# Kernel tuning notes

Measured on AMD Instinct MI355X. Metric: run time of the kernel, lower is better.

Reference implementation:

```python
import jax, jax.numpy as jnp
import numpy as np

B, L, ENC_IN, C_OUT = 4, 2048, 64, 64
D_MODEL, N_HEADS, D_FF, E_LAYERS = 1024, 16, 4096, 4
CA_K = 5  # ChannelAttention1D kernel: int(|log2(1024)+1|/2)=5 (odd)


def _layer_norm(x, w, b, eps=1e-5):
    m = x.mean(-1, keepdims=True)
    v = ((x - m) ** 2).mean(-1, keepdims=True)
    return (x - m) * jax.lax.rsqrt(v + eps) * w + b


def _flow_attention(q, k, v):
    # q,k,v: [B, L, H, D] -> work in [B, H, L, D]
    q = jax.nn.sigmoid(jnp.swapaxes(q, 1, 2))
    k = jax.nn.sigmoid(jnp.swapaxes(k, 1, 2))
    v = jnp.swapaxes(v, 1, 2)
    eps = 1e-6
    Lq = q.shape[2]
    S = k.shape[2]
    nr = 1.0 / jnp.einsum('bhld,bhd->bhl', q + eps, k.sum(axis=2) + eps)
    nc = 1.0 / jnp.einsum('bhsd,bhd->bhs', k + eps, q.sum(axis=2) + eps)
    nrr = jnp.einsum('bhld,bhd->bhl', q + eps, (k * nc[..., None]).sum(axis=2) + eps)
    ncr = jnp.einsum('bhsd,bhd->bhs', k + eps, (q * nr[..., None]).sum(axis=2) + eps)
    nrr = jax.nn.sigmoid(nrr * (float(Lq) / float(S)))
    ncr = jax.nn.softmax(ncr, axis=-1) * S
    kv = jnp.einsum('bhsd,bhse->bhde', k, v * ncr[..., None])  # [B,H,D,Dv]
    out = jnp.einsum('bhld,bhde->bhle', q, kv) * nr[..., None] * nrr[..., None]
    return jnp.swapaxes(out, 1, 2)  # [B, L, H, Dv]


def _token_embed(x, w):
    # x: [B, L, Cin]; circular conv1d kernel=3, pad=1, no bias
    xt = jnp.swapaxes(x, 1, 2)  # [B, Cin, L]
    xt = jnp.concatenate([xt[..., -1:], xt, xt[..., :1]], axis=-1)
    y = jax.lax.conv_general_dilated(xt, w, (1,), 'VALID',
                                     dimension_numbers=('NCH', 'OIH', 'NCH'))
    return jnp.swapaxes(y, 1, 2)  # [B, L, d_model]


def _channel_att(x, w):
    # x: [B, L, C]; squeeze over L, conv over channel axis, sigmoid gate
    y = x.mean(axis=1, keepdims=True)  # [B, 1, C]
    pad = CA_K // 2
    yp = jnp.pad(y, ((0, 0), (0, 0), (pad, pad)))
    yc = jax.lax.conv_general_dilated(yp, w.reshape(1, 1, CA_K), (1,), 'VALID',
                                      dimension_numbers=('NCH', 'OIH', 'NCH'))
    return x * jax.nn.sigmoid(yc)


def _encoder_layer(x, Wq, bq, Wk, bk, Wv, bv, Wo, bo,
                   ln1w, ln1b, ln2w, ln2b, c1w, c1b, c2w, c2b):
    Bx, Lx, _ = x.shape
    q = (x @ Wq.T + bq).reshape(Bx, Lx, N_HEADS, -1)
    k = (x @ Wk.T + bk).reshape(Bx, Lx, N_HEADS, -1)
    v = (x @ Wv.T + bv).reshape(Bx, Lx, N_HEADS, -1)
    a = _flow_attention(q, k, v).reshape(Bx, Lx, -1)
    a = a @ Wo.T + bo
    x = _layer_norm(x + a, ln1w, ln1b)
    y = jax.nn.relu(jnp.einsum('bld,fd->blf', x, c1w) + c1b)  # conv1 k=1
    y = jnp.einsum('blf,df->bld', y, c2w) + c2b               # conv2 k=1
    return _layer_norm(x + y, ln2w, ln2b)


def setup_inputs() -> dict:
    key = jax.random.key(0)
    ks = jax.random.split(key, 16)
    s = 0.02
    E, D, F = E_LAYERS, D_MODEL, D_FF
    inp = {
        'x': jax.random.normal(ks[0], (B, L, ENC_IN), jnp.float32),
        'tok_conv_w': jax.random.normal(ks[1], (D, ENC_IN, 3), jnp.float32) * s,
        'Wq': jax.random.normal(ks[2], (E, D, D), jnp.float32) * s,
        'bq': jnp.zeros((E, D), jnp.float32),
        'Wk': jax.random.normal(ks[3], (E, D, D), jnp.float32) * s,
        'bk': jnp.zeros((E, D), jnp.float32),
        'Wv': jax.random.normal(ks[4], (E, D, D), jnp.float32) * s,
        'bv': jnp.zeros((E, D), jnp.float32),
        'Wo': jax.random.normal(ks[5], (E, D, D), jnp.float32) * s,
        'bo': jnp.zeros((E, D), jnp.float32),
        'conv1_w': jax.random.normal(ks[6], (E, F, D), jnp.float32) * s,
        'conv1_b': jnp.zeros((E, F), jnp.float32),
        'conv2_w': jax.random.normal(ks[7], (E, D, F), jnp.float32) * s,
        'conv2_b': jnp.zeros((E, D), jnp.float32),
        'ln1_w': jnp.ones((E, D), jnp.float32),
        'ln1_b': jnp.zeros((E, D), jnp.float32),
        'ln2_w': jnp.ones((E, D), jnp.float32),
        'ln2_b': jnp.zeros((E, D), jnp.float32),
        'ca_w': jax.random.normal(ks[8], (E, CA_K), jnp.float32) * 0.2,
        'lnf_w': jnp.ones((D,), jnp.float32),
        'lnf_b': jnp.zeros((D,), jnp.float32),
        'proj_w': jax.random.normal(ks[9], (C_OUT, D), jnp.float32) * s,
        'proj_b': jnp.zeros((C_OUT,), jnp.float32),
    }
    return inp


def reference(x, tok_conv_w, Wq, bq, Wk, bk, Wv, bv, Wo, bo,
              conv1_w, conv1_b, conv2_w, conv2_b,
              ln1_w, ln1_b, ln2_w, ln2_b, ca_w,
              lnf_w, lnf_b, proj_w, proj_b):
    h = _token_embed(x, tok_conv_w)  # dropout = identity (eval)
    for i in range(E_LAYERS):
        h = _encoder_layer(h, Wq[i], bq[i], Wk[i], bk[i], Wv[i], bv[i], Wo[i], bo[i],
                           ln1_w[i], ln1_b[i], ln2_w[i], ln2_b[i],
                           conv1_w[i], conv1_b[i], conv2_w[i], conv2_b[i])
        h = _channel_att(h, ca_w[i])
    # Encoder re-applies the last attention layer after the conv loop (faithful)
    i = E_LAYERS - 1
    h = _encoder_layer(h, Wq[i], bq[i], Wk[i], bk[i], Wv[i], bv[i], Wo[i], bo[i],
                       ln1_w[i], ln1_b[i], ln2_w[i], ln2_b[i],
                       conv1_w[i], conv1_b[i], conv2_w[i], conv2_b[i])
    h = _layer_norm(h, lnf_w, lnf_b)
    return h @ proj_w.T + proj_b
```

## Files before the change

### kernel.cpp

```cpp
#include <hip/hip_runtime.h>
#include <stdint.h>

#define L_SEQ 2048
#define DM 1024
#define NH 16
#define DFF 4096
#define NB 4
#define ROWS (NB * L_SEQ)

typedef __attribute__((ext_vector_type(8))) __bf16 bf16x8;
typedef __attribute__((ext_vector_type(4))) float f32x4;

__device__ __forceinline__ float bf2f(unsigned short u) {
  union { unsigned int i; float f; } x; x.i = ((unsigned int)u) << 16; return x.f;
}
__device__ __forceinline__ unsigned short f2bf(float f) {
  union { float f; unsigned int i; } x; x.f = f;
  unsigned int r = x.i + 0x7FFFu + ((x.i >> 16) & 1u);
  return (unsigned short)(r >> 16);
}

typedef __attribute__((address_space(3))) void lds_void;
typedef const __attribute__((address_space(1))) void gbl_void;

__device__ __forceinline__ void stage16(const void* g, void* ldsbase) {
  __builtin_amdgcn_global_load_lds((gbl_void*)g, (lds_void*)ldsbase, 16, 0, 0);
}

__global__ __launch_bounds__(256)
void gemm_bt(const unsigned short* __restrict__ A,
             const unsigned short* __restrict__ B,
             const float* __restrict__ bias,
             unsigned short* __restrict__ C16,
             float* __restrict__ C32,
             int K, int lda, int ldc, int n_limit, int act)
{
  __shared__ __attribute__((aligned(16))) unsigned short As[128 * 32];
  __shared__ __attribute__((aligned(16))) unsigned short Bs[128 * 32];
  const int tid  = threadIdx.x;
  const int wave = tid >> 6, lane = tid & 63;
  const int wm = (wave & 1) << 6, wn = (wave >> 1) << 6;
  const int l16 = lane & 15, quad = lane >> 4;

  const unsigned short* Ab = A + (size_t)blockIdx.x * 128 * lda;
  const unsigned short* Bb = B + (size_t)blockIdx.y * 128 * K;

  const int srow = (wave << 4) + (lane >> 2);
  const int scol = (lane & 3) << 3;

  f32x4 acc[4][4] = {};

  for (int k0 = 0; k0 < K; k0 += 32) {
    const size_t aoff = (size_t)srow * lda + k0 + scol;
    const size_t boff = (size_t)srow * K   + k0 + scol;
    stage16(Ab + aoff,                    &As[(wave * 16) * 32]);
    stage16(Ab + aoff + (size_t)64 * lda, &As[(wave * 16 + 64) * 32]);
    stage16(Bb + boff,                    &Bs[(wave * 16) * 32]);
    stage16(Bb + boff + (size_t)64 * K,   &Bs[(wave * 16 + 64) * 32]);
    __syncthreads();

    bf16x8 af[4], bfr[4];
#pragma unroll
    for (int mi = 0; mi < 4; mi++)
      af[mi] = *(const bf16x8*)&As[(wm + mi * 16 + l16) * 32 + quad * 8];
#pragma unroll
    for (int ni = 0; ni < 4; ni++)
      bfr[ni] = *(const bf16x8*)&Bs[(wn + ni * 16 + l16) * 32 + quad * 8];
#pragma unroll
    for (int mi = 0; mi < 4; mi++)
#pragma unroll
      for (int ni = 0; ni < 4; ni++)
        acc[mi][ni] = __builtin_amdgcn_mfma_f32_16x16x32_bf16(af[mi], bfr[ni], acc[mi][ni], 0, 0, 0);
    __syncthreads();
  }

  const int row0 = (int)blockIdx.x * 128 + wm + quad * 4;
  const int col0 = (int)blockIdx.y * 128 + wn + l16;
#pragma unroll
  for (int ni = 0; ni < 4; ni++) {
    const int col = col0 + ni * 16;
    if (col >= n_limit) continue;
    const float bv = bias ? bias[col] : 0.0f;
    const bool sig = (act == 2) || (act == 3 && col < 2048);
#pragma unroll
    for (int mi = 0; mi < 4; mi++) {
#pragma unroll
      for (int r = 0; r < 4; r++) {
        const int row = row0 + mi * 16 + r;
        float v = acc[mi][ni][r] + bv;
        if (act == 1) v = fmaxf(v, 0.0f);
        else if (sig) v = 1.0f / (1.0f + __expf(-v));
        if (C32) C32[(size_t)row * ldc + col] = v;
        if (C16) C16[(size_t)row * ldc + col] = f2bf(v);
      }
    }
  }
}


__global__ __launch_bounds__(256)
void fa_sums(const unsigned short* __restrict__ Q, const unsigned short* __restrict__ K,
             int ld, float* __restrict__ ksp, float* __restrict__ qsp)
{
  const int bh = blockIdx.x, chunk = blockIdx.y;
  const size_t base = ((size_t)(bh >> 4) * L_SEQ) * ld + (size_t)(bh & 15) * 64;
  const int t = threadIdx.x, lane = t & 63, wave = t >> 6;
  __shared__ float red[256];
  float ks = 0.f, qs = 0.f;
  const int l0 = chunk * 256 + wave * 64;
  for (int i = 0; i < 64; i++) {
    const size_t idx = base + (size_t)(l0 + i) * ld + lane;
    ks += bf2f(K[idx]);
    qs += bf2f(Q[idx]);
  }
  red[t] = ks; __syncthreads();
  if (t < 64) ksp[(bh * 8 + chunk) * 64 + t] = red[t] + red[t + 64] + red[t + 128] + red[t + 192];
  __syncthreads();
  red[t] = qs; __syncthreads();
  if (t < 64) qsp[(bh * 8 + chunk) * 64 + t] = red[t] + red[t + 64] + red[t + 128] + red[t + 192];
}

__global__ __launch_bounds__(256)
void fa_rows1(const unsigned short* __restrict__ Q, const unsigned short* __restrict__ K,
              int ld, const float* __restrict__ ksp, const float* __restrict__ qsp,
              float* __restrict__ nr, float* __restrict__ t1p, float* __restrict__ t2p)
{
  const int bh = blockIdx.x, chunk = blockIdx.y;
  const size_t base = ((size_t)(bh >> 4) * L_SEQ) * ld + (size_t)(bh & 15) * 64;
  const int t = threadIdx.x, lane = t & 63, wave = t >> 6;
  const float eps = 1e-6f;
  __shared__ float s_kse[64], s_qse[64], red[256];
  if (t < 64) {
    float s = 0.f;
    for (int j = 0; j < 8; j++) s += ksp[(bh * 8 + j) * 64 + t];
    s_kse[t] = s + eps;
  } else if (t < 128) {
    const int d = t - 64;
    float s = 0.f;
    for (int j = 0; j < 8; j++) s += qsp[(bh * 8 + j) * 64 + d];
    s_qse[d] = s + eps;
  }
  __syncthreads();
  const float kse = s_kse[lane], qse = s_qse[lane];
  float t1a = 0.f, t2a = 0.f;
  for (int i = 0; i < 32; i++) {
    const int l = chunk * 128 + wave + 4 * i;
    const size_t idx = base + (size_t)l * ld + lane;
    const float q = bf2f(Q[idx]), k = bf2f(K[idx]);
    float a = (q + eps) * kse;
    float c = (k + eps) * qse;
#pragma unroll
    for (int off = 32; off; off >>= 1) { a += __shfl_xor(a, off); c += __shfl_xor(c, off); }
    const float nrl = 1.f / a, ncl = 1.f / c;
    if (lane == 0) nr[bh * L_SEQ + l] = nrl;
    t1a += k * ncl;
    t2a += q * nrl;
  }
  red[t] = t1a; __syncthreads();
  if (t < 64) t1p[(bh * 16 + chunk) * 64 + t] = red[t] + red[t + 64] + red[t + 128] + red[t + 192];
  __syncthreads();
  red[t] = t2a; __syncthreads();
  if (t < 64) t2p[(bh * 16 + chunk) * 64 + t] = red[t] + red[t + 64] + red[t + 128] + red[t + 192];
}

__global__ __launch_bounds__(256)
void fa_rows2(const unsigned short* __restrict__ Q, const unsigned short* __restrict__ K,
              int ld, const float* __restrict__ t1p, const float* __restrict__ t2p,
              float* __restrict__ nr, float* __restrict__ sc)
{
  const int bh = blockIdx.x, chunk = blockIdx.y;
  const size_t base = ((size_t)(bh >> 4) * L_SEQ) * ld + (size_t)(bh & 15) * 64;
  const int t = threadIdx.x, lane = t & 63, wave = t >> 6;
  const float eps = 1e-6f;
  __shared__ float s_t1e[64], s_t2e[64];
  if (t < 64) {
    float s = 0.f;
    for (int j = 0; j < 16; j++) s += t1p[(bh * 16 + j) * 64 + t];
    s_t1e[t] = s + eps;
  } else if (t < 128) {
    const int d = t - 64;
    float s = 0.f;
    for (int j = 0; j < 16; j++) s += t2p[(bh * 16 + j) * 64 + d];
    s_t2e[d] = s + eps;
  }
  __syncthreads();
  const float t1e = s_t1e[lane], t2e = s_t2e[lane];
  for (int i = 0; i < 32; i++) {
    const int l = chunk * 128 + wave + 4 * i;
    const size_t idx = base + (size_t)l * ld + lane;
    const float q = bf2f(Q[idx]), k = bf2f(K[idx]);
    float a = (q + eps) * t1e;
    float c = (k + eps) * t2e;
#pragma unroll
    for (int off = 32; off; off >>= 1) { a += __shfl_xor(a, off); c += __shfl_xor(c, off); }
    if (lane == 0) {
      nr[bh * L_SEQ + l] *= 1.f / (1.f + __expf(-a));
      sc[bh * L_SEQ + l] = c;
    }
  }
}

__global__ __launch_bounds__(256)
void fa_softmax(float* __restrict__ sc, float* __restrict__ kv)
{
  const int bh = blockIdx.x, t = threadIdx.x;
  __shared__ float red[256];
  float4* kvz = (float4*)(kv + bh * 64 * 64);
  for (int j = 0; j < 4; j++) kvz[t + 256 * j] = make_float4(0.f, 0.f, 0.f, 0.f);

  float* row = sc + bh * L_SEQ;
  float m = -3.4e38f;
  for (int l = t; l < L_SEQ; l += 256) m = fmaxf(m, row[l]);
  red[t] = m; __syncthreads();
  for (int s = 128; s > 0; s >>= 1) { if (t < s) red[t] = fmaxf(red[t], red[t + s]); __syncthreads(); }
  const float mx = red[0];
  __syncthreads();
  float ps = 0.f;
  float pv[8];
#pragma unroll
  for (int j = 0; j < 8; j++) {
    const int l = t + 256 * j;
    pv[j] = __expf(row[l] - mx);
    ps += pv[j];
  }
  red[t] = ps; __syncthreads();
  for (int s = 128; s > 0; s >>= 1) { if (t < s) red[t] += red[t + s]; __syncthreads(); }
  const float scale = (float)L_SEQ / red[0];
#pragma unroll
  for (int j = 0; j < 8; j++) row[t + 256 * j] = pv[j] * scale;
}

__global__ __launch_bounds__(256)
void fa_kv(const unsigned short* __restrict__ K, const unsigned short* __restrict__ V,
           int ld, const float* __restrict__ sc, float* __restrict__ kv)
{
  const int bh = blockIdx.x, chunk = blockIdx.y;
  const size_t base = ((size_t)(bh >> 4) * L_SEQ) * ld + (size_t)(bh & 15) * 64;
  const int t = threadIdx.x, lane = t & 63, wave = t >> 6;
  const int l16 = lane & 15, quad = lane >> 4;
  __shared__ __attribute__((aligned(16))) unsigned short s_kT[64 * 72];
  __shared__ __attribute__((aligned(16))) unsigned short s_vT[64 * 72];

  f32x4 acc5[4] = {};
  for (int sub = 0; sub < 2; sub++) {
    const int l0 = chunk * 128 + sub * 64;
#pragma unroll
    for (int it = 0; it < 4; it++) {
      const int task = it * 256 + t;
      const int l = task >> 4;
      const int g = task & 15;
      const size_t gidx = base + (size_t)(l0 + l) * ld + g * 4;
      const ushort4 k4 = *(const ushort4*)(K + gidx);
      const ushort4 v4 = *(const ushort4*)(V + gidx);
      const float wgt = sc[bh * L_SEQ + l0 + l];
      s_kT[(g * 4 + 0) * 72 + l] = k4.x;
      s_kT[(g * 4 + 1) * 72 + l] = k4.y;
      s_kT[(g * 4 + 2) * 72 + l] = k4.z;
      s_kT[(g * 4 + 3) * 72 + l] = k4.w;
      s_vT[(g * 4 + 0) * 72 + l] = f2bf(bf2f(v4.x) * wgt);
      s_vT[(g * 4 + 1) * 72 + l] = f2bf(bf2f(v4.y) * wgt);
      s_vT[(g * 4 + 2) * 72 + l] = f2bf(bf2f(v4.z) * wgt);
      s_vT[(g * 4 + 3) * 72 + l] = f2bf(bf2f(v4.w) * wgt);
    }
    __syncthreads();
#pragma unroll
    for (int ks = 0; ks < 2; ks++) {
      const bf16x8 af = *(const bf16x8*)&s_kT[(wave * 16 + l16) * 72 + ks * 32 + quad * 8];
#pragma unroll
      for (int et = 0; et < 4; et++) {
        const bf16x8 bf = *(const bf16x8*)&s_vT[(et * 16 + l16) * 72 + ks * 32 + quad * 8];
        acc5[et] = __builtin_amdgcn_mfma_f32_16x16x32_bf16(af, bf, acc5[et], 0, 0, 0);
      }
    }
    __syncthreads();
  }
#pragma unroll
  for (int et = 0; et < 4; et++)
#pragma unroll
    for (int r = 0; r < 4; r++)
      atomicAdd(&kv[bh * 4096 + (wave * 16 + quad * 4 + r) * 64 + et * 16 + l16], acc5[et][r]);
}

__global__ __launch_bounds__(256)
void fa_out(const unsigned short* __restrict__ Q, int ld, const float* __restrict__ kv,
            const float* __restrict__ nr, unsigned short* O)
{
  const int bh = blockIdx.x, chunk = blockIdx.y;
  const size_t base = ((size_t)(bh >> 4) * L_SEQ) * ld + (size_t)(bh & 15) * 64;
  const int t = threadIdx.x, lane = t & 63, wave = t >> 6;
  const int l16 = lane & 15, quad = lane >> 4;
  __shared__ __attribute__((aligned(16))) unsigned short s_kvT[64 * 72];

#pragma unroll
  for (int j = 0; j < 16; j++) {
    const int i = t + 256 * j;
    const int d = i >> 6, e = i & 63;
    s_kvT[e * 72 + d] = f2bf(kv[bh * 4096 + i]);
  }
  __syncthreads();

  bf16x8 bfr6[4][2];
#pragma unroll
  for (int et = 0; et < 4; et++)
#pragma unroll
    for (int ks = 0; ks < 2; ks++)
      bfr6[et][ks] = *(const bf16x8*)&s_kvT[(et * 16 + l16) * 72 + ks * 32 + quad * 8];

#pragma unroll
  for (int ti = 0; ti < 2; ti++) {
    const int l0 = chunk * 128 + (wave * 2 + ti) * 16;
    f32x4 oc[4] = {};
#pragma unroll
    for (int ks = 0; ks < 2; ks++) {
      const bf16x8 aq = *(const bf16x8*)(Q + base + (size_t)(l0 + l16) * ld + ks * 32 + quad * 8);
#pragma unroll
      for (int et = 0; et < 4; et++)
        oc[et] = __builtin_amdgcn_mfma_f32_16x16x32_bf16(aq, bfr6[et][ks], oc[et], 0, 0, 0);
    }
#pragma unroll
    for (int r = 0; r < 4; r++) {
      const int l = l0 + quad * 4 + r;
      const float scl = nr[bh * L_SEQ + l];
#pragma unroll
      for (int et = 0; et < 4; et++)
        O[base + (size_t)l * ld + et * 16 + l16] = f2bf(oc[et][r] * scl);
    }
  }
}

__global__ __launch_bounds__(256)
void ln_fused(const float* res, const float* __restrict__ add,
              const float* __restrict__ w, const float* __restrict__ bb,
              float* out32, unsigned short* out16)
{
  const int row = blockIdx.x * 4 + (threadIdx.x >> 6);
  const int lane = threadIdx.x & 63;
  const size_t roff = (size_t)row * DM;
  const float4* rp = (const float4*)(res + roff);
  const float4* ap = add ? (const float4*)(add + roff) : nullptr;

  float x[16], s = 0.f, s2 = 0.f;
#pragma unroll
  for (int q4 = 0; q4 < 4; q4++) {
    float4 v = rp[lane * 4 + q4];
    if (ap) { float4 a = ap[lane * 4 + q4]; v.x += a.x; v.y += a.y; v.z += a.z; v.w += a.w; }
    x[q4 * 4 + 0] = v.x; x[q4 * 4 + 1] = v.y; x[q4 * 4 + 2] = v.z; x[q4 * 4 + 3] = v.w;
    s += v.x + v.y + v.z + v.w;
    s2 += v.x * v.x + v.y * v.y + v.z * v.z + v.w * v.w;
  }
#pragma unroll
  for (int off = 32; off; off >>= 1) { s += __shfl_xor(s, off); s2 += __shfl_xor(s2, off); }
  const float mean = s * (1.f / DM);
  const float var = s2 * (1.f / DM) - mean * mean;
  const float rstd = rsqrtf(var + 1e-5f);
#pragma unroll
  for (int j = 0; j < 16; j++) {
    const int c = lane * 16 + j;
    x[j] = (x[j] - mean) * rstd * w[c] + bb[c];
  }
  if (out32) {
    float4* op = (float4*)(out32 + roff);
#pragma unroll
    for (int q4 = 0; q4 < 4; q4++) {
      float4 v; v.x = x[q4*4+0]; v.y = x[q4*4+1]; v.z = x[q4*4+2]; v.w = x[q4*4+3];
      op[lane * 4 + q4] = v;
    }
  }
  if (out16) {
#pragma unroll
    for (int q4 = 0; q4 < 4; q4++) {
      ushort4 u;
      u.x = f2bf(x[q4*4+0]); u.y = f2bf(x[q4*4+1]); u.z = f2bf(x[q4*4+2]); u.w = f2bf(x[q4*4+3]);
      *(ushort4*)(out16 + roff + lane * 16 + q4 * 4) = u;
    }
  }
}

__global__ void ca_zero(float* __restrict__ ybar) {
  const int i = blockIdx.x * 256 + threadIdx.x;
  if (i < NB * DM) ybar[i] = 0.f;
}
__global__ void ca_mean(const unsigned short* __restrict__ H16, float* __restrict__ ybar) {
  const int b = blockIdx.x, cc = blockIdx.y, lc = blockIdx.z;
  const int c = cc * 256 + threadIdx.x;
  float s = 0.f;
  for (int l = lc * 256; l < lc * 256 + 256; l++)
    s += bf2f(H16[((size_t)(b * L_SEQ + l)) * DM + c]);
  atomicAdd(&ybar[b * DM + c], s);
}
__global__ void ca_gate(const float* __restrict__ ybar, const float* __restrict__ cw,
                        float* __restrict__ gate) {
  const int i = blockIdx.x * 256 + threadIdx.x;
  if (i >= NB * DM) return;
  const int b = i >> 10, c = i & 1023;
  float acc = 0.f;
#pragma unroll
  for (int j = 0; j < 5; j++) {
    const int cc = c + j - 2;
    const float yv = (cc >= 0 && cc < DM) ? ybar[b * DM + cc] * (1.f / L_SEQ) : 0.f;
    acc += cw[j] * yv;
  }
  gate[i] = 1.f / (1.f + __expf(-acc));
}
__global__ void ca_apply(float* __restrict__ H32, unsigned short* __restrict__ H16,
                         const float* __restrict__ gate) {
  const size_t i = ((size_t)blockIdx.x * 256 + threadIdx.x) * 4;
  const int row = (int)(i >> 10);
  const int b = row >> 11;
  const int c = (int)(i & 1023);
  float4 v = *(float4*)(H32 + i);
  v.x *= gate[b * DM + c + 0];
  v.y *= gate[b * DM + c + 1];
  v.z *= gate[b * DM + c + 2];
  v.w *= gate[b * DM + c + 3];
  *(float4*)(H32 + i) = v;
  unsigned short* hp = H16 + i;
  hp[0] = f2bf(v.x); hp[1] = f2bf(v.y); hp[2] = f2bf(v.z); hp[3] = f2bf(v.w);
}

__global__ void embed_gather(const float* __restrict__ x, unsigned short* __restrict__ Ae) {
  const int i = blockIdx.x * 256 + threadIdx.x;
  if (i >= ROWS * 192) return;
  const int row = i / 192, kk = i % 192;
  const int t3 = kk >> 6, c = kk & 63;
  const int b = row >> 11, l = row & 2047;
  const int ls = (l + t3 - 1 + L_SEQ) & 2047;
  Ae[i] = f2bf(x[((size_t)(b * L_SEQ + ls)) * 64 + c]);
}
__global__ void embed_repack(const float* __restrict__ w, unsigned short* __restrict__ We) {
  const int i = blockIdx.x * 256 + threadIdx.x;
  if (i >= DM * 192) return;
  const int f = i / 192, kk = i % 192;
  const int t3 = kk >> 6, c = kk & 63;
  We[i] = f2bf(w[(f * 64 + c) * 3 + t3]);
}
__global__ void pad_proj(const float* __restrict__ pw, unsigned short* __restrict__ Wp) {
  const int i = blockIdx.x * 256 + threadIdx.x;
  if (i >= 128 * DM) return;
  Wp[i] = ((i >> 10) < 64) ? f2bf(pw[i]) : (unsigned short)0;
}
__global__ void pack_qkv_bias(const float* __restrict__ bq, const float* __restrict__ bk,
                              const float* __restrict__ bv, float* __restrict__ bqkv) {
  const int i = blockIdx.x * 256 + threadIdx.x;
  if (i >= 3072) return;
  bqkv[i] = (i < 1024) ? bq[i] : (i < 2048 ? bk[i - 1024] : bv[i - 2048]);
}
__global__ void cvt_layer_weights(const float* __restrict__ Wq, const float* __restrict__ Wk,
                                  const float* __restrict__ Wv, const float* __restrict__ Wo,
                                  const float* __restrict__ c1, const float* __restrict__ c2,
                                  unsigned short* __restrict__ Wl, unsigned short* __restrict__ WlFF) {
  const int g = blockIdx.x * 256 + threadIdx.x;
  const int i = g << 2;
  const float* src; unsigned short* dst;
  if (i < (1 << 22)) {
    const int w = i >> 20, off = i & ((1 << 20) - 1);
    const float* srcs[4] = {Wq, Wk, Wv, Wo};
    src = srcs[w] + off; dst = Wl + (w << 20) + off;
  } else {
    const int j = i - (1 << 22);
    const int w = j >> 22, off = j & ((1 << 22) - 1);
    src = (w ? c2 : c1) + off; dst = WlFF + (w << 22) + off;
  }
  const float4 v = *(const float4*)src;
  ushort4 u; u.x = f2bf(v.x); u.y = f2bf(v.y); u.z = f2bf(v.z); u.w = f2bf(v.w);
  *(ushort4*)dst = u;
}

extern "C" void kernel_launch(void* const* d_in, const int* in_sizes, int n_in,
                              void* d_out, int out_size, void* d_ws, size_t ws_size,
                              hipStream_t stream) {
  const float* x     = (const float*)d_in[0];
  const float* tokw  = (const float*)d_in[1];
  const float* Wq    = (const float*)d_in[2];
  const float* bq    = (const float*)d_in[3];
  const float* Wk    = (const float*)d_in[4];
  const float* bk    = (const float*)d_in[5];
  const float* Wv    = (const float*)d_in[6];
  const float* bv    = (const float*)d_in[7];
  const float* Wo    = (const float*)d_in[8];
  const float* bo    = (const float*)d_in[9];
  const float* c1w   = (const float*)d_in[10];
  const float* c1b   = (const float*)d_in[11];
  const float* c2w   = (const float*)d_in[12];
  const float* c2b   = (const float*)d_in[13];
  const float* ln1w  = (const float*)d_in[14];
  const float* ln1b  = (const float*)d_in[15];
  const float* ln2w  = (const float*)d_in[16];
  const float* ln2b  = (const float*)d_in[17];
  const float* caw   = (const float*)d_in[18];
  const float* lnfw  = (const float*)d_in[19];
  const float* lnfb  = (const float*)d_in[20];
  const float* projw = (const float*)d_in[21];
  const float* projb = (const float*)d_in[22];

  char* ws = (char*)d_ws;
  float*          R32 = (float*)(ws);
  unsigned short* R16 = (unsigned short*)(ws + ((size_t)32 << 20));
  float*          A32 = (float*)(ws + ((size_t)48 << 20));
  unsigned short* U   = (unsigned short*)(ws + ((size_t)80 << 20));
  unsigned short* QKV16 = U;
  unsigned short* F16   = U;
  char* fa = ws + ((size_t)128 << 20);
  float* fa_nr  = (float*)(fa);
  float* fa_sc  = (float*)(fa + (512 << 10));
  float* fa_ksp = (float*)(fa + (1024 << 10));
  float* fa_qsp = (float*)(fa + (1152 << 10));
  float* fa_t1p = (float*)(fa + (1280 << 10));
  float* fa_t2p = (float*)(fa + (1792 << 10));
  float* fa_kvb = (float*)(fa + (2304 << 10));
  unsigned short* Wl   = (unsigned short*)(ws + ((size_t)144 << 20));
  unsigned short* WlFF = (unsigned short*)(ws + ((size_t)152 << 20));
  char* misc = ws + ((size_t)168 << 20);
  float*          ybar = (float*)misc;
  float*          gate = (float*)(misc + (16 << 10));
  float*          bqkv = (float*)(misc + (32 << 10));
  unsigned short* We   = (unsigned short*)(misc + (64 << 10));
  unsigned short* Wp   = (unsigned short*)(misc + (512 << 10));

  const int BIG = 1 << 30;
  auto gemm = [&](const unsigned short* A, const unsigned short* B, const float* bias,
                  unsigned short* C16, float* C32, int N, int K, int lda, int ldc,
                  int nlim, int act) {
    dim3 grid(ROWS / 128, N / 128);
    gemm_bt<<<grid, dim3(256), 0, stream>>>(A, B, bias, C16, C32, K, lda, ldc, nlim, act);
  };

  embed_gather<<<(ROWS * 192 + 255) / 256, 256, 0, stream>>>(x, U);
  embed_repack<<<(DM * 192 + 255) / 256, 256, 0, stream>>>(tokw, We);
  gemm(U, We, nullptr, R16, R32, DM, 192, 192, DM, BIG, 0);

  for (int it = 0; it < 5; it++) {
    const int i = (it < 4) ? it : 3;
    if (it != 4) {
      cvt_layer_weights<<<(3 << 20) / 256, 256, 0, stream>>>(
          Wq + ((size_t)i << 20), Wk + ((size_t)i << 20),
          Wv + ((size_t)i << 20), Wo + ((size_t)i << 20),
          c1w + ((size_t)i << 22), c2w + ((size_t)i << 22), Wl, WlFF);
      pack_qkv_bias<<<12, 256, 0, stream>>>(bq + i * DM, bk + i * DM, bv + i * DM, bqkv);
    }
    const unsigned short* Wo16 = Wl + (3 << 20);
    const unsigned short* C116 = WlFF;
    const unsigned short* C216 = WlFF + (1 << 22);

    gemm(R16, Wl, bqkv, QKV16, nullptr, 3072, DM, DM, 3072, BIG, 3);

    const unsigned short* Qp = QKV16;
    const unsigned short* Kp = QKV16 + 1024;
    unsigned short*       Vp = QKV16 + 2048;

    fa_sums   <<<dim3(64, 8),  256, 0, stream>>>(Qp, Kp, 3072, fa_ksp, fa_qsp);
    fa_rows1  <<<dim3(64, 16), 256, 0, stream>>>(Qp, Kp, 3072, fa_ksp, fa_qsp, fa_nr, fa_t1p, fa_t2p);
    fa_rows2  <<<dim3(64, 16), 256, 0, stream>>>(Qp, Kp, 3072, fa_t1p, fa_t2p, fa_nr, fa_sc);
    fa_softmax<<<dim3(64),     256, 0, stream>>>(fa_sc, fa_kvb);
    fa_kv     <<<dim3(64, 16), 256, 0, stream>>>(Kp, Vp, 3072, fa_sc, fa_kvb);
    fa_out    <<<dim3(64, 16), 256, 0, stream>>>(Qp, 3072, fa_kvb, fa_nr, Vp);

    gemm(Vp, Wo16, bo + i * DM, nullptr, A32, DM, DM, 3072, DM, BIG, 0);
    ln_fused<<<ROWS / 4, 256, 0, stream>>>(R32, A32, ln1w + i * DM, ln1b + i * DM, R32, R16);
    gemm(R16, C116, c1b + i * DFF, F16, nullptr, DFF, DM, DM, DFF, BIG, 1);
    gemm(F16, C216, c2b + i * DM, nullptr, A32, DM, DFF, DFF, DM, BIG, 0);
    ln_fused<<<ROWS / 4, 256, 0, stream>>>(R32, A32, ln2w + i * DM, ln2b + i * DM, R32, R16);

    if (it < 4) {
      ca_zero<<<16, 256, 0, stream>>>(ybar);
      ca_mean<<<dim3(NB, 4, 8), 256, 0, stream>>>(R16, ybar);
      ca_gate<<<16, 256, 0, stream>>>(ybar, caw + i * 5, gate);
      ca_apply<<<(ROWS * DM / 4) / 256, 256, 0, stream>>>(R32, R16, gate);
    }
  }

  ln_fused<<<ROWS / 4, 256, 0, stream>>>(R32, nullptr, lnfw, lnfb, nullptr, U);
  pad_proj<<<(128 * DM + 255) / 256, 256, 0, stream>>>(projw, Wp);
  gemm(U, Wp, projb, nullptr, (float*)d_out, 128, DM, DM, 64, 64, 0);

  (void)in_sizes; (void)n_in; (void)out_size; (void)ws_size;
}
```

Before: 2.826 ms.

## Add 256x256-tile 8-wave GEMM with double-buffered LDS and XCD-aware block remap

Adds a gemm256 kernel that computes 256x256 output tiles with 512 threads. It double-buffers K=64 slices in 128KB of LDS, interleaves global staging with MFMA phases using barriers and setprio, and remaps block IDs so neighbouring tiles land on the same XCD. The dispatcher routes GEMMs with N divisible by 256 and K divisible by 64 to the new kernel, which covers all the large projection and FFN GEMMs. The aim is more data reuse per LDS load and better overlap of memory with compute. In exchange it uses more registers and LDS per block and launches fewer blocks.

Measured after the change: 3.159 ms. 1.12x slower.

```diff
diff --git a/kernel.cpp b/kernel.cpp
--- a/kernel.cpp
+++ b/kernel.cpp
@@ -88,6 +88,151 @@
       for (int r = 0; r < 4; r++) {
         const int row = row0 + mi * 16 + r;
         float v = acc[mi][ni][r] + bv;
+        if (act == 1) v = fmaxf(v, 0.0f);
+        else if (sig) v = 1.0f / (1.0f + __expf(-v));
+        if (C32) C32[(size_t)row * ldc + col] = v;
+        if (C16) C16[(size_t)row * ldc + col] = f2bf(v);
+      }
+    }
+  }
+}
+
+#define AFRAG(bb, mi, ks) (*(const bf16x8*)(smb + (bb) + ((mi) << 11) + ((ks) << 10) + lb))
+#define BFRAG(bb, nj, ks) (*(const bf16x8*)(smb + (bb) + 32768 + ((nj) << 11) + ((ks) << 10) + lb))
+
+#define LOAD_A(bb, qm) \
+  fa[0][0] = AFRAG(bb, wm8 + (qm)*4 + 0, 0); fa[0][1] = AFRAG(bb, wm8 + (qm)*4 + 0, 1); \
+  fa[1][0] = AFRAG(bb, wm8 + (qm)*4 + 1, 0); fa[1][1] = AFRAG(bb, wm8 + (qm)*4 + 1, 1); \
+  fa[2][0] = AFRAG(bb, wm8 + (qm)*4 + 2, 0); fa[2][1] = AFRAG(bb, wm8 + (qm)*4 + 2, 1); \
+  fa[3][0] = AFRAG(bb, wm8 + (qm)*4 + 3, 0); fa[3][1] = AFRAG(bb, wm8 + (qm)*4 + 3, 1);
+
+#define LOAD_B(bb, qn) \
+  fb[(qn)*2+0][0] = BFRAG(bb, wn4 + (qn)*2 + 0, 0); fb[(qn)*2+0][1] = BFRAG(bb, wn4 + (qn)*2 + 0, 1); \
+  fb[(qn)*2+1][0] = BFRAG(bb, wn4 + (qn)*2 + 1, 0); fb[(qn)*2+1][1] = BFRAG(bb, wn4 + (qn)*2 + 1, 1);
+
+#define MM(mi, nj) \
+  acc[mi][nj] = __builtin_amdgcn_mfma_f32_16x16x32_bf16(fa[(mi)&3][0], fb[nj][0], acc[mi][nj], 0, 0, 0); \
+  acc[mi][nj] = __builtin_amdgcn_mfma_f32_16x16x32_bf16(fa[(mi)&3][1], fb[nj][1], acc[mi][nj], 0, 0, 0);
+
+#define MFMA_QUAD(qm, qn) \
+  MM((qm)*4+0, (qn)*2+0) MM((qm)*4+0, (qn)*2+1) \
+  MM((qm)*4+1, (qn)*2+0) MM((qm)*4+1, (qn)*2+1) \
+  MM((qm)*4+2, (qn)*2+0) MM((qm)*4+2, (qn)*2+1) \
+  MM((qm)*4+3, (qn)*2+0) MM((qm)*4+3, (qn)*2+1)
+
+#define PH_MFMA(qm, qn) \
+  __builtin_amdgcn_s_barrier(); \
+  asm volatile("s_waitcnt lgkmcnt(0)" ::: "memory"); \
+  __builtin_amdgcn_sched_barrier(0); \
+  __builtin_amdgcn_s_setprio(1); \
+  MFMA_QUAD(qm, qn); \
+  __builtin_amdgcn_s_setprio(0); \
+  __builtin_amdgcn_sched_barrier(0); \
+  __builtin_amdgcn_s_barrier();
+
+__global__ __launch_bounds__(512, 2)
+void gemm256(const unsigned short* __restrict__ A,
+             const unsigned short* __restrict__ B,
+             const float* __restrict__ bias,
+             unsigned short* __restrict__ C16,
+             float* __restrict__ C32,
+             int K, int lda, int ldc, int n_limit, int act, int nb)
+{
+  __shared__ __attribute__((aligned(16))) unsigned short sm[65536];
+  char* smb = (char*)sm;
+
+  const int tid  = threadIdx.x;
+  const int wave = tid >> 6, lane = tid & 63;
+  const int l16 = lane & 15, quad = lane >> 4;
+  const int lb = lane << 4;
+  const int wm = wave >> 2, wn = wave & 3;
+  const int wm8 = wm * 8, wn4 = wn * 4;
+
+  const int nwg  = (int)gridDim.x;
+  const int orig = (int)blockIdx.x;
+  const int qq = nwg >> 3, rr = nwg & 7;
+  const int xcd = orig & 7, loc = orig >> 3;
+  const int wgid = (xcd < rr ? xcd * (qq + 1) : rr * (qq + 1) + (xcd - rr) * qq) + loc;
+  const int bx = wgid / nb, by = wgid % nb;
+
+  const unsigned short* Ab = A + (size_t)bx * 256 * lda;
+  const unsigned short* Bb = B + (size_t)by * 256 * K;
+
+  const int rb0 = ((wave >> 1) << 4) + l16;
+  const int cb0 = ((wave & 1) << 5) + (quad << 3);
+
+  const int T = K >> 6;
+
+  auto stageHalf = [&](int bufbyte, int h, int t) {
+    const unsigned short* src;
+    size_t ld;
+    if (h < 2) { ld = (size_t)lda; src = Ab + (size_t)((h & 1) * 128 + rb0) * ld + (size_t)t * 64 + cb0; }
+    else       { ld = (size_t)K;   src = Bb + (size_t)((h & 1) * 128 + rb0) * ld + (size_t)t * 64 + cb0; }
+    char* dst = smb + bufbyte + h * 16384 + wave * 1024;
+    stage16(src, dst);
+    stage16(src + 64 * ld, dst + 8192);
+  };
+
+  bf16x8 fa[4][2], fb[4][2];
+  f32x4 acc[8][4] = {};
+
+  stageHalf(0, 0, 0); stageHalf(0, 1, 0); stageHalf(0, 2, 0); stageHalf(0, 3, 0);
+  if (T > 1) {
+    stageHalf(1 << 16, 0, 1);
+    asm volatile("s_waitcnt vmcnt(2)" ::: "memory");
+  } else {
+    asm volatile("s_waitcnt vmcnt(0)" ::: "memory");
+  }
+  __builtin_amdgcn_sched_barrier(0);
+  __builtin_amdgcn_s_barrier();
+
+  for (int t = 0; t < T; ++t) {
+    const int bb  = (t & 1) << 16;
+    const int nbb = bb ^ (1 << 16);
+    const bool st1 = (t + 1 < T), st2 = (t + 2 < T);
+
+    LOAD_A(bb, 0)
+    LOAD_B(bb, 0)
+    if (st1) stageHalf(nbb, 1, t + 1);
+    PH_MFMA(0, 0)
+
+    LOAD_B(bb, 1)
+    if (st1) stageHalf(nbb, 2, t + 1);
+    PH_MFMA(0, 1)
+
+    LOAD_A(bb, 1)
+    if (st1) stageHalf(nbb, 3, t + 1);
+    PH_MFMA(1, 1)
+
+    if (st2) {
+      stageHalf(bb, 0, t + 2);
+      asm volatile("s_waitcnt vmcnt(2)" ::: "memory");
+    } else {
+      asm volatile("s_waitcnt vmcnt(0)" ::: "memory");
+    }
+    __builtin_amdgcn_sched_barrier(0);
+    __builtin_amdgcn_s_barrier();
+    __builtin_amdgcn_s_setprio(1);
+    MFMA_QUAD(1, 0)
+    __builtin_amdgcn_s_setprio(0);
+    __builtin_amdgcn_sched_barrier(0);
+    __builtin_amdgcn_s_barrier();
+  }
+
+  const int row0 = bx * 256 + wm * 128 + quad * 4;
+  const int col0 = by * 256 + wn * 64 + l16;
+#pragma unroll
+  for (int nj = 0; nj < 4; ++nj) {
+    const int col = col0 + nj * 16;
+    if (col >= n_limit) continue;
+    const float bv = bias ? bias[col] : 0.0f;
+    const bool sig = (act == 2) || (act == 3 && col < 2048);
+#pragma unroll
+    for (int mi = 0; mi < 8; ++mi) {
+#pragma unroll
+      for (int r = 0; r < 4; ++r) {
+        const int row = row0 + mi * 16 + r;
+        float v = acc[mi][nj][r] + bv;
         if (act == 1) v = fmaxf(v, 0.0f);
         else if (sig) v = 1.0f / (1.0f + __expf(-v));
         if (C32) C32[(size_t)row * ldc + col] = v;
@@ -521,8 +666,14 @@
   auto gemm = [&](const unsigned short* A, const unsigned short* B, const float* bias,
                   unsigned short* C16, float* C32, int N, int K, int lda, int ldc,
                   int nlim, int act) {
-    dim3 grid(ROWS / 128, N / 128);
-    gemm_bt<<<grid, dim3(256), 0, stream>>>(A, B, bias, C16, C32, K, lda, ldc, nlim, act);
+    if ((N & 255) == 0 && (K & 63) == 0) {
+      const int nb = N >> 8;
+      const int nwg = (ROWS >> 8) * nb;
+      gemm256<<<dim3(nwg), dim3(512), 0, stream>>>(A, B, bias, C16, C32, K, lda, ldc, nlim, act, nb);
+    } else {
+      dim3 grid(ROWS / 128, N / 128);
+      gemm_bt<<<grid, dim3(256), 0, stream>>>(A, B, bias, C16, C32, K, lda, ldc, nlim, act);
+    }
   };
 
   embed_gather<<<(ROWS * 192 + 255) / 256, 256, 0, stream>>>(x, U);
```

## Restructure GEMM with fragment-ordered LDS, 64-wide K tiles and XCD-aware block mapping

Applied to the files above, without the earlier changes.

The GEMM kernel now stages 16-byte chunks into LDS in the exact order the MFMA fragments are read. This makes each lane's fragment load a contiguous, conflict-free access. The K step doubles to 64, which halves the number of barrier pairs per tile. The 2D grid is flattened and remapped so consecutive tiles land on the same XCD, to improve L2 reuse, and launch bounds request 4 blocks per CU. The kernel now assumes K is a multiple of 64 and uses 32 KB of LDS per block, which may limit occupancy.

Measured after the change: 3.253 ms. 15.1% more time.

```diff
diff --git a/kernel.cpp b/kernel.cpp
--- a/kernel.cpp
+++ b/kernel.cpp
@@ -27,67 +27,82 @@
   __builtin_amdgcn_global_load_lds((gbl_void*)g, (lds_void*)ldsbase, 16, 0, 0);
 }
 
-__global__ __launch_bounds__(256)
-void gemm_bt(const unsigned short* __restrict__ A,
-             const unsigned short* __restrict__ B,
-             const float* __restrict__ bias,
-             unsigned short* __restrict__ C16,
-             float* __restrict__ C32,
-             int K, int lda, int ldc, int n_limit, int act)
-{
-  __shared__ __attribute__((aligned(16))) unsigned short As[128 * 32];
-  __shared__ __attribute__((aligned(16))) unsigned short Bs[128 * 32];
+#define MFMA1(d, a, b) (d) = __builtin_amdgcn_mfma_f32_16x16x32_bf16((a), (b), (d), 0, 0, 0)
+
+__global__ __launch_bounds__(256, 4)
+void gemm_f(const unsigned short* __restrict__ A,
+            const unsigned short* __restrict__ B,
+            const float* __restrict__ bias,
+            unsigned short* __restrict__ C16,
+            float* __restrict__ C32,
+            int K, int lda, int ldc, int n_limit, int act, int nb)
+{
+  __shared__ __attribute__((aligned(16))) unsigned short sm[16384];
+  char* smb = (char*)sm;
   const int tid  = threadIdx.x;
   const int wave = tid >> 6, lane = tid & 63;
-  const int wm = (wave & 1) << 6, wn = (wave >> 1) << 6;
   const int l16 = lane & 15, quad = lane >> 4;
-
-  const unsigned short* Ab = A + (size_t)blockIdx.x * 128 * lda;
-  const unsigned short* Bb = B + (size_t)blockIdx.y * 128 * K;
-
-  const int srow = (wave << 4) + (lane >> 2);
-  const int scol = (lane & 3) << 3;
+  const int lb = lane << 4;
+  const int wm = wave >> 1, wn = wave & 1;
+
+  const int nwg  = (int)gridDim.x;
+  const int orig = (int)blockIdx.x;
+  const int qq = nwg >> 3, rr = nwg & 7;
+  const int xcd = orig & 7, loc = orig >> 3;
+  const int wgid = (xcd < rr ? xcd * (qq + 1) : rr * (qq + 1) + (xcd - rr) * qq) + loc;
+  const int bx = wgid / nb, by = wgid % nb;
+
+  const unsigned short* Ab = A + (size_t)bx * 128 * lda;
+  const unsigned short* Bb = B + (size_t)by * 128 * K;
+
+  const int rb0 = ((wave >> 1) << 4) + l16;
+  const int cb0 = ((wave & 1) << 5) + (quad << 3);
 
   f32x4 acc[4][4] = {};
-
-  for (int k0 = 0; k0 < K; k0 += 32) {
-    const size_t aoff = (size_t)srow * lda + k0 + scol;
-    const size_t boff = (size_t)srow * K   + k0 + scol;
-    stage16(Ab + aoff,                    &As[(wave * 16) * 32]);
-    stage16(Ab + aoff + (size_t)64 * lda, &As[(wave * 16 + 64) * 32]);
-    stage16(Bb + boff,                    &Bs[(wave * 16) * 32]);
-    stage16(Bb + boff + (size_t)64 * K,   &Bs[(wave * 16 + 64) * 32]);
+  const int T = K >> 6;
+
+  for (int t = 0; t < T; ++t) {
+    const unsigned short* sa = Ab + (size_t)rb0 * lda + t * 64 + cb0;
+    const unsigned short* sb = Bb + (size_t)rb0 * K   + t * 64 + cb0;
+    char* da = smb + wave * 1024;
+    char* db = smb + 16384 + wave * 1024;
+#pragma unroll
+    for (int j = 0; j < 4; ++j) {
+      stage16(sa + (size_t)(j * 32) * lda, da + j * 4096);
+      stage16(sb + (size_t)(j * 32) * K,   db + j * 4096);
+    }
     __syncthreads();
-
-    bf16x8 af[4], bfr[4];
-#pragma unroll
-    for (int mi = 0; mi < 4; mi++)
-      af[mi] = *(const bf16x8*)&As[(wm + mi * 16 + l16) * 32 + quad * 8];
-#pragma unroll
-    for (int ni = 0; ni < 4; ni++)
-      bfr[ni] = *(const bf16x8*)&Bs[(wn + ni * 16 + l16) * 32 + quad * 8];
-#pragma unroll
-    for (int mi = 0; mi < 4; mi++)
-#pragma unroll
-      for (int ni = 0; ni < 4; ni++)
-        acc[mi][ni] = __builtin_amdgcn_mfma_f32_16x16x32_bf16(af[mi], bfr[ni], acc[mi][ni], 0, 0, 0);
+#pragma unroll
+    for (int ks = 0; ks < 2; ++ks) {
+      bf16x8 af[4], bf[4];
+#pragma unroll
+      for (int i = 0; i < 4; ++i) {
+        af[i] = *(const bf16x8*)(smb + ((((wm * 4 + i) * 2 + ks)) << 10) + lb);
+        bf[i] = *(const bf16x8*)(smb + 16384 + ((((wn * 4 + i) * 2 + ks)) << 10) + lb);
+      }
+#pragma unroll
+      for (int i = 0; i < 4; ++i)
+#pragma unroll
+        for (int j = 0; j < 4; ++j)
+          MFMA1(acc[i][j], af[i], bf[j]);
+    }
     __syncthreads();
   }
 
-  const int row0 = (int)blockIdx.x * 128 + wm + quad * 4;
-  const int col0 = (int)blockIdx.y * 128 + wn + l16;
-#pragma unroll
-  for (int ni = 0; ni < 4; ni++) {
-    const int col = col0 + ni * 16;
+  const int row0 = bx * 128 + wm * 64 + quad * 4;
+  const int col0 = by * 128 + wn * 64 + l16;
+#pragma unroll
+  for (int nj = 0; nj < 4; ++nj) {
+    const int col = col0 + nj * 16;
     if (col >= n_limit) continue;
     const float bv = bias ? bias[col] : 0.0f;
     const bool sig = (act == 2) || (act == 3 && col < 2048);
 #pragma unroll
-    for (int mi = 0; mi < 4; mi++) {
-#pragma unroll
-      for (int r = 0; r < 4; r++) {
+    for (int mi = 0; mi < 4; ++mi) {
+#pragma unroll
+      for (int r = 0; r < 4; ++r) {
         const int row = row0 + mi * 16 + r;
-        float v = acc[mi][ni][r] + bv;
+        float v = acc[mi][nj][r] + bv;
         if (act == 1) v = fmaxf(v, 0.0f);
         else if (sig) v = 1.0f / (1.0f + __expf(-v));
         if (C32) C32[(size_t)row * ldc + col] = v;
@@ -521,8 +536,9 @@
   auto gemm = [&](const unsigned short* A, const unsigned short* B, const float* bias,
                   unsigned short* C16, float* C32, int N, int K, int lda, int ldc,
                   int nlim, int act) {
-    dim3 grid(ROWS / 128, N / 128);
-    gemm_bt<<<grid, dim3(256), 0, stream>>>(A, B, bias, C16, C32, K, lda, ldc, nlim, act);
+    const int nb = N >> 7;
+    gemm_f<<<dim3((ROWS >> 7) * nb), dim3(256), 0, stream>>>(
+        A, B, bias, C16, C32, K, lda, ldc, nlim, act, nb);
   };
 
   embed_gather<<<(ROWS * 192 + 255) / 256, 256, 0, stream>>>(x, U);
```
